# Optimization experiments

Hardware: AMD Instinct MI355X
Metric: run time of the kernel (lower is better)

Reference implementation:

```python
import jax, jax.numpy as jnp
import numpy as np

NUM_EXPERTS = 8
TOP_K = 2


def setup_inputs() -> dict:
    key = jax.random.key(0)
    ks = jax.random.split(key, 5)
    B, S, D, F, E = 4, 2048, 1024, 3584, NUM_EXPERTS
    scale = 0.02
    return {
        "hidden_states": jax.random.normal(ks[0], (B, S, D), dtype=jnp.float32),
        "gate_w": jax.random.normal(ks[1], (E, D), dtype=jnp.float32) * scale,
        "w1": jax.random.normal(ks[2], (E, D, F), dtype=jnp.float32) * scale,
        "w3": jax.random.normal(ks[3], (E, D, F), dtype=jnp.float32) * scale,
        "w2": jax.random.normal(ks[4], (E, F, D), dtype=jnp.float32) * scale,
    }


def reference(hidden_states, gate_w, w1, w3, w2):
    B, S, D = hidden_states.shape
    E = gate_w.shape[0]
    x = hidden_states.reshape(-1, D)  # [T, D]

    # Router: logits -> softmax -> top-k -> renormalize
    router_logits = x @ gate_w.T  # [T, E]
    routing_probs = jax.nn.softmax(router_logits, axis=-1)
    top_w, top_idx = jax.lax.top_k(routing_probs, TOP_K)  # [T, K]
    top_w = top_w / jnp.sum(top_w, axis=-1, keepdims=True)

    # Per-token weight for each expert (0 if not selected): [T, E]
    expert_weight = jnp.sum(
        jax.nn.one_hot(top_idx, E, dtype=x.dtype) * top_w[..., None], axis=1
    )

    # Dense masked dispatch: small fixed loop over experts (E=8), SwiGLU MLP.
    out = jnp.zeros_like(x)
    for e in range(E):
        h = jax.nn.silu(x @ w1[e]) * (x @ w3[e])  # [T, F]
        out = out + expert_weight[:, e:e + 1] * (h @ w2[e])  # [T, D]

    return out.reshape(B, S, D), router_logits
```

## Files before the change

kernel.cpp:

```cpp
#include <hip/hip_runtime.h>
#include <stdint.h>

#define T_TOKENS 8192
#define DDIM 1024
#define FDIM 3584
#define NEXP 8

#define BM 128
#define BK 64
#define MAXRT (T_TOKENS / BM)
#define H_ROWS (2 * T_TOKENS + BM)

typedef _Float16 f16x8 __attribute__((ext_vector_type(8)));
typedef _Float16 f16x4 __attribute__((ext_vector_type(4)));
typedef float f32x4 __attribute__((ext_vector_type(4)));

__device__ __forceinline__ void gload16(const void* g, void* l) {
  __builtin_amdgcn_global_load_lds(
      (const __attribute__((address_space(1))) void*)g,
      (__attribute__((address_space(3))) void*)l, 16, 0, 0);
}

__global__ __launch_bounds__(256) void router_kernel(
    const float* __restrict__ x, const float* __restrict__ gw,
    float* __restrict__ logits_out, int* __restrict__ counts,
    int* __restrict__ tok_idx, float* __restrict__ tok_w) {
  int t = blockIdx.x * 4 + (threadIdx.x >> 6);
  int lane = threadIdx.x & 63;
  const float* xr = x + (size_t)t * DDIM;
  float acc[NEXP];
#pragma unroll
  for (int e = 0; e < NEXP; e++) acc[e] = 0.f;
  for (int c = 0; c < DDIM / 64; c++) {
    float xv = xr[c * 64 + lane];
#pragma unroll
    for (int e = 0; e < NEXP; e++) acc[e] += xv * gw[e * DDIM + c * 64 + lane];
  }
#pragma unroll
  for (int e = 0; e < NEXP; e++) {
    for (int off = 32; off > 0; off >>= 1) acc[e] += __shfl_xor(acc[e], off, 64);
  }
  if (lane == 0) {
    float m = acc[0];
    for (int e = 1; e < NEXP; e++) m = fmaxf(m, acc[e]);
    float p[NEXP];
    for (int e = 0; e < NEXP; e++) p[e] = expf(acc[e] - m);
    int e1 = 0;
    for (int e = 1; e < NEXP; e++) if (p[e] > p[e1]) e1 = e;
    int e2 = (e1 == 0) ? 1 : 0;
    for (int e = 0; e < NEXP; e++) { if (e == e1) continue; if (p[e] > p[e2]) e2 = e; }
    float wsum = p[e1] + p[e2];
    float w1v = p[e1] / wsum, w2v = p[e2] / wsum;
    for (int e = 0; e < NEXP; e++) logits_out[(size_t)t * NEXP + e] = acc[e];
    int pos1 = atomicAdd(&counts[e1], 1);
    tok_idx[e1 * T_TOKENS + pos1] = t; tok_w[e1 * T_TOKENS + pos1] = w1v;
    int pos2 = atomicAdd(&counts[e2], 1);
    tok_idx[e2 * T_TOKENS + pos2] = t; tok_w[e2 * T_TOKENS + pos2] = w2v;
  }
}

__global__ void prefix_kernel(const int* __restrict__ counts, int* __restrict__ offsets) {
  if (threadIdx.x == 0) {
    int s = 0;
    for (int e = 0; e < NEXP; e++) { offsets[e] = s; s += counts[e]; }
    offsets[NEXP] = s;
  }
}

__global__ __launch_bounds__(256) void convert_x_kernel(const float* __restrict__ x,
                                                        _Float16* __restrict__ xh) {
  int i = blockIdx.x * 256 + threadIdx.x;
  const float4* s = (const float4*)x + (size_t)i * 2;
  float4 a = s[0], b = s[1];
  f16x8 o = {(_Float16)a.x, (_Float16)a.y, (_Float16)a.z, (_Float16)a.w,
             (_Float16)b.x, (_Float16)b.y, (_Float16)b.z, (_Float16)b.w};
  *((f16x8*)xh + i) = o;
}

__global__ __launch_bounds__(256) void transpose_f16_kernel(
    const float* __restrict__ in, _Float16* __restrict__ out, int R, int C) {
  __shared__ _Float16 lt[64][72];
  size_t esz = (size_t)R * C;
  in += blockIdx.z * esz;
  out += blockIdx.z * esz;
  int r0 = blockIdx.y * 64, c0 = blockIdx.x * 64;
  int t = threadIdx.x;
  int r = t >> 2, cs = (t & 3) * 16;
  const float* src = in + (size_t)(r0 + r) * C + c0 + cs;
#pragma unroll
  for (int q = 0; q < 4; q++) {
    float4 v = ((const float4*)src)[q];
    lt[cs + q * 4 + 0][r] = (_Float16)v.x;
    lt[cs + q * 4 + 1][r] = (_Float16)v.y;
    lt[cs + q * 4 + 2][r] = (_Float16)v.z;
    lt[cs + q * 4 + 3][r] = (_Float16)v.w;
  }
  __syncthreads();
  int cl = t >> 2, rs = (t & 3) * 16;
  _Float16* dst = out + (size_t)(c0 + cl) * R + r0 + rs;
#pragma unroll
  for (int q = 0; q < 2; q++)
    *(f16x8*)(dst + q * 8) = *(const f16x8*)&lt[cl][rs + q * 8];
}

__global__ __launch_bounds__(256) void gemm1_kernel(
    const _Float16* __restrict__ xh, const _Float16* __restrict__ w1t,
    const _Float16* __restrict__ w3t, const int* __restrict__ counts,
    const int* __restrict__ offsets, const int* __restrict__ tok_idx,
    _Float16* __restrict__ h) {
  int e = blockIdx.z;
  int cnt = counts[e];
  int rt = blockIdx.y;
  if (rt * BM >= cnt) return;
  int ct = blockIdx.x;
  int off = offsets[e];

  __shared__ _Float16 lA[BM * 64];
  __shared__ _Float16 lB1[64 * 64];
  __shared__ _Float16 lB3[64 * 64];

  int tid = threadIdx.x, lane = tid & 63, w = tid >> 6;
  int p = lane & 7;
  int rsub = lane >> 3;
  int c = p ^ rsub;

  const _Float16* aG[4];
  _Float16* aL[4];
#pragma unroll
  for (int g = 0; g < 4; g++) {
    int r = w * 32 + g * 8 + rsub;
    int ir = rt * BM + r;
    if (ir >= cnt) ir = cnt - 1;
    int tok = tok_idx[e * T_TOKENS + ir];
    aG[g] = xh + (size_t)tok * DDIM + c * 8;
    aL[g] = lA + (w * 32 + g * 8) * 64;
  }
  const _Float16 *b1G[2], *b3G[2];
  _Float16 *b1L[2], *b3L[2];
#pragma unroll
  for (int g = 0; g < 2; g++) {
    int n = w * 16 + g * 8 + rsub;
    size_t row = (size_t)e * FDIM + (size_t)ct * 64 + n;
    b1G[g] = w1t + row * DDIM + c * 8;
    b3G[g] = w3t + row * DDIM + c * 8;
    b1L[g] = lB1 + (w * 16 + g * 8) * 64;
    b3L[g] = lB3 + (w * 16 + g * 8) * 64;
  }

  f32x4 acc1[2][4], acc3[2][4];
  f32x4 zero = {0.f, 0.f, 0.f, 0.f};
#pragma unroll
  for (int i = 0; i < 2; i++)
#pragma unroll
    for (int j = 0; j < 4; j++) { acc1[i][j] = zero; acc3[i][j] = zero; }

  int wm = w * 32;
  int l15 = lane & 15;
  int qv = lane >> 4;
  int x7 = l15 & 7;

  for (int kt = 0; kt < DDIM / BK; kt++) {
#pragma unroll
    for (int g = 0; g < 4; g++) { gload16(aG[g], aL[g]); aG[g] += 64; }
#pragma unroll
    for (int g = 0; g < 2; g++) {
      gload16(b1G[g], b1L[g]); b1G[g] += 64;
      gload16(b3G[g], b3L[g]); b3G[g] += 64;
    }
    __syncthreads();
#pragma unroll
    for (int kk = 0; kk < 2; kk++) {
      int pc = (kk * 4 + qv) ^ x7;
      f16x8 af[2], b1f[4], b3f[4];
#pragma unroll
      for (int i = 0; i < 2; i++)
        af[i] = *(const f16x8*)&lA[(wm + i * 16 + l15) * 64 + pc * 8];
#pragma unroll
      for (int j = 0; j < 4; j++) {
        b1f[j] = *(const f16x8*)&lB1[(j * 16 + l15) * 64 + pc * 8];
        b3f[j] = *(const f16x8*)&lB3[(j * 16 + l15) * 64 + pc * 8];
      }
#pragma unroll
      for (int i = 0; i < 2; i++)
#pragma unroll
        for (int j = 0; j < 4; j++) {
          acc1[i][j] = __builtin_amdgcn_mfma_f32_16x16x32_f16(af[i], b1f[j], acc1[i][j], 0, 0, 0);
          acc3[i][j] = __builtin_amdgcn_mfma_f32_16x16x32_f16(af[i], b3f[j], acc3[i][j], 0, 0, 0);
        }
    }
    __syncthreads();
  }
  int q4 = qv * 4;
#pragma unroll
  for (int i = 0; i < 2; i++) {
#pragma unroll
    for (int r = 0; r < 4; r++) {
      int row = rt * BM + wm + i * 16 + q4 + r;
      if (row >= cnt) continue;
      _Float16* hrow = h + (size_t)(off + row) * FDIM + (size_t)ct * 64;
#pragma unroll
      for (int j = 0; j < 4; j++) {
        float a = acc1[i][j][r];
        float b = acc3[i][j][r];
        float hv = (a / (1.f + __expf(-a))) * b;
        hrow[j * 16 + l15] = (_Float16)hv;
      }
    }
  }
}

__global__ __launch_bounds__(256) void gemm2_kernel(
    const _Float16* __restrict__ h, const _Float16* __restrict__ w2t,
    const int* __restrict__ counts, const int* __restrict__ offsets,
    const int* __restrict__ tok_idx, const float* __restrict__ tok_w,
    float* __restrict__ out) {
  int e = blockIdx.z;
  int cnt = counts[e];
  int rt = blockIdx.y;
  if (rt * BM >= cnt) return;
  int ct = blockIdx.x;
  int off = offsets[e];

  __shared__ _Float16 lA[BM * 64];
  __shared__ _Float16 lB[128 * 64];

  int tid = threadIdx.x, lane = tid & 63, w = tid >> 6;
  int p = lane & 7;
  int rsub = lane >> 3;
  int c = p ^ rsub;

  const _Float16 *aG[4], *bG[4];
  _Float16 *aL[4], *bL[4];
#pragma unroll
  for (int g = 0; g < 4; g++) {
    int r = w * 32 + g * 8 + rsub;
    aG[g] = h + (size_t)(off + rt * BM + r) * FDIM + c * 8;
    aL[g] = lA + (w * 32 + g * 8) * 64;
    size_t row = (size_t)e * DDIM + (size_t)ct * 128 + r;
    bG[g] = w2t + row * FDIM + c * 8;
    bL[g] = lB + (w * 32 + g * 8) * 64;
  }

  f32x4 acc[2][8];
  f32x4 zero = {0.f, 0.f, 0.f, 0.f};
#pragma unroll
  for (int i = 0; i < 2; i++)
#pragma unroll
    for (int j = 0; j < 8; j++) acc[i][j] = zero;

  int wm = w * 32;
  int l15 = lane & 15;
  int qv = lane >> 4;
  int x7 = l15 & 7;

  for (int kt = 0; kt < FDIM / BK; kt++) {
#pragma unroll
    for (int g = 0; g < 4; g++) {
      gload16(aG[g], aL[g]); aG[g] += 64;
      gload16(bG[g], bL[g]); bG[g] += 64;
    }
    __syncthreads();
#pragma unroll
    for (int kk = 0; kk < 2; kk++) {
      int pc = (kk * 4 + qv) ^ x7;
      f16x8 af[2], bf[8];
#pragma unroll
      for (int i = 0; i < 2; i++)
        af[i] = *(const f16x8*)&lA[(wm + i * 16 + l15) * 64 + pc * 8];
#pragma unroll
      for (int j = 0; j < 8; j++)
        bf[j] = *(const f16x8*)&lB[(j * 16 + l15) * 64 + pc * 8];
#pragma unroll
      for (int i = 0; i < 2; i++)
#pragma unroll
        for (int j = 0; j < 8; j++)
          acc[i][j] = __builtin_amdgcn_mfma_f32_16x16x32_f16(af[i], bf[j], acc[i][j], 0, 0, 0);
    }
    __syncthreads();
  }
  int q4 = qv * 4;
#pragma unroll
  for (int i = 0; i < 2; i++) {
#pragma unroll
    for (int r = 0; r < 4; r++) {
      int row = rt * BM + wm + i * 16 + q4 + r;
      if (row >= cnt) continue;
      int t = tok_idx[e * T_TOKENS + row];
      float wgt = tok_w[e * T_TOKENS + row];
      float* orow = out + (size_t)t * DDIM + (size_t)ct * 128;
#pragma unroll
      for (int j = 0; j < 8; j++)
        atomicAdd(&orow[j * 16 + l15], acc[i][j][r] * wgt);
    }
  }
}

extern "C" void kernel_launch(void* const* d_in, const int* in_sizes, int n_in,
                              void* d_out, int out_size, void* d_ws, size_t ws_size,
                              hipStream_t stream) {
  const float* x  = (const float*)d_in[0];
  const float* gw = (const float*)d_in[1];
  const float* w1 = (const float*)d_in[2];
  const float* w3 = (const float*)d_in[3];
  const float* w2 = (const float*)d_in[4];
  float* out = (float*)d_out;
  float* logits = out + (size_t)T_TOKENS * DDIM;

  char* ws = (char*)d_ws;
  const size_t MB = 1024 * 1024;
  int* counts  = (int*)ws;
  int* offsets = (int*)(ws + 64);
  int* tok_idx = (int*)(ws + 256);
  float* tok_w = (float*)(ws + 256 + (size_t)NEXP * T_TOKENS * 4);
  _Float16* xh  = (_Float16*)(ws + 1 * MB);
  _Float16* w1t = (_Float16*)(ws + 17 * MB);
  _Float16* w3t = (_Float16*)(ws + 73 * MB);
  _Float16* w2t = (_Float16*)(ws + 129 * MB);
  _Float16* h   = (_Float16*)(ws + 185 * MB);

  hipMemsetAsync(counts, 0, 256, stream);
  hipMemsetAsync(out, 0, (size_t)T_TOKENS * DDIM * 4, stream);

  convert_x_kernel<<<T_TOKENS * DDIM / 8 / 256, 256, 0, stream>>>(x, xh);
  transpose_f16_kernel<<<dim3(FDIM / 64, DDIM / 64, NEXP), 256, 0, stream>>>(w1, w1t, DDIM, FDIM);
  transpose_f16_kernel<<<dim3(FDIM / 64, DDIM / 64, NEXP), 256, 0, stream>>>(w3, w3t, DDIM, FDIM);
  transpose_f16_kernel<<<dim3(DDIM / 64, FDIM / 64, NEXP), 256, 0, stream>>>(w2, w2t, FDIM, DDIM);

  router_kernel<<<T_TOKENS / 4, 256, 0, stream>>>(x, gw, logits, counts, tok_idx, tok_w);
  prefix_kernel<<<1, 64, 0, stream>>>(counts, offsets);

  gemm1_kernel<<<dim3(FDIM / 64, MAXRT, NEXP), 256, 0, stream>>>(xh, w1t, w3t, counts, offsets, tok_idx, h);
  gemm2_kernel<<<dim3(DDIM / 128, MAXRT, NEXP), 256, 0, stream>>>(h, w2t, counts, offsets, tok_idx, tok_w, out);
}
```

Before: 1.149 ms.

## Compact MoE tile schedule, replace atomic scatter with fp16 partials plus gather

Builds a compact list of (expert, row-tile) pairs in the prefix kernel, so the GEMM grids launch only up to 136 tiles instead of 8x64 mostly-empty blocks. Replaces per-element float atomicAdd scatter in gemm2 with fp16 partial rows written per assignment, then a gather kernel sums each token's two contributions. This also removes the output memset. Fuses the x-to-fp16 conversion into the router and reworks the transpose thread mapping. The partial sums are rounded to fp16 before the final add, which adds precision loss, plus an extra pass over the partial buffer.

New measurement: 1.140 ms. No clear change (-0.8%).

```diff
diff --git a/kernel.cpp b/kernel.cpp
--- a/kernel.cpp
+++ b/kernel.cpp
@@ -8,11 +8,9 @@
 
 #define BM 128
 #define BK 64
-#define MAXRT (T_TOKENS / BM)
-#define H_ROWS (2 * T_TOKENS + BM)
+#define MAXTT 136
 
 typedef _Float16 f16x8 __attribute__((ext_vector_type(8)));
-typedef _Float16 f16x4 __attribute__((ext_vector_type(4)));
 typedef float f32x4 __attribute__((ext_vector_type(4)));
 
 __device__ __forceinline__ void gload16(const void* g, void* l) {
@@ -24,7 +22,8 @@
 __global__ __launch_bounds__(256) void router_kernel(
     const float* __restrict__ x, const float* __restrict__ gw,
     float* __restrict__ logits_out, int* __restrict__ counts,
-    int* __restrict__ tok_idx, float* __restrict__ tok_w) {
+    int* __restrict__ tok_idx, float* __restrict__ tok_w,
+    int2* __restrict__ tok_ref, _Float16* __restrict__ xh) {
   int t = blockIdx.x * 4 + (threadIdx.x >> 6);
   int lane = threadIdx.x & 63;
   const float* xr = x + (size_t)t * DDIM;
@@ -33,6 +32,7 @@
   for (int e = 0; e < NEXP; e++) acc[e] = 0.f;
   for (int c = 0; c < DDIM / 64; c++) {
     float xv = xr[c * 64 + lane];
+    xh[(size_t)t * DDIM + c * 64 + lane] = (_Float16)xv;
 #pragma unroll
     for (int e = 0; e < NEXP; e++) acc[e] += xv * gw[e * DDIM + c * 64 + lane];
   }
@@ -56,62 +56,62 @@
     tok_idx[e1 * T_TOKENS + pos1] = t; tok_w[e1 * T_TOKENS + pos1] = w1v;
     int pos2 = atomicAdd(&counts[e2], 1);
     tok_idx[e2 * T_TOKENS + pos2] = t; tok_w[e2 * T_TOKENS + pos2] = w2v;
-  }
-}
-
-__global__ void prefix_kernel(const int* __restrict__ counts, int* __restrict__ offsets) {
+    tok_ref[t] = make_int2((e1 << 13) | pos1, (e2 << 13) | pos2);
+  }
+}
+
+__global__ void prefix_kernel(const int* __restrict__ counts, int* __restrict__ offsets,
+                              int* __restrict__ sched) {
   if (threadIdx.x == 0) {
-    int s = 0;
-    for (int e = 0; e < NEXP; e++) { offsets[e] = s; s += counts[e]; }
+    int s = 0, nt = 0;
+    for (int e = 0; e < NEXP; e++) {
+      offsets[e] = s;
+      int c = counts[e];
+      int ntile = (c + BM - 1) / BM;
+      for (int i = 0; i < ntile; i++) sched[nt++] = (e << 16) | i;
+      s += c;
+    }
     offsets[NEXP] = s;
-  }
-}
-
-__global__ __launch_bounds__(256) void convert_x_kernel(const float* __restrict__ x,
-                                                        _Float16* __restrict__ xh) {
-  int i = blockIdx.x * 256 + threadIdx.x;
-  const float4* s = (const float4*)x + (size_t)i * 2;
-  float4 a = s[0], b = s[1];
-  f16x8 o = {(_Float16)a.x, (_Float16)a.y, (_Float16)a.z, (_Float16)a.w,
-             (_Float16)b.x, (_Float16)b.y, (_Float16)b.z, (_Float16)b.w};
-  *((f16x8*)xh + i) = o;
+    for (; nt < MAXTT; nt++) sched[nt] = -1;
+  }
 }
 
 __global__ __launch_bounds__(256) void transpose_f16_kernel(
     const float* __restrict__ in, _Float16* __restrict__ out, int R, int C) {
   __shared__ _Float16 lt[64][72];
   size_t esz = (size_t)R * C;
-  in += blockIdx.z * esz;
-  out += blockIdx.z * esz;
+  in += (size_t)blockIdx.z * esz;
+  out += (size_t)blockIdx.z * esz;
   int r0 = blockIdx.y * 64, c0 = blockIdx.x * 64;
   int t = threadIdx.x;
-  int r = t >> 2, cs = (t & 3) * 16;
-  const float* src = in + (size_t)(r0 + r) * C + c0 + cs;
-#pragma unroll
-  for (int q = 0; q < 4; q++) {
-    float4 v = ((const float4*)src)[q];
-    lt[cs + q * 4 + 0][r] = (_Float16)v.x;
-    lt[cs + q * 4 + 1][r] = (_Float16)v.y;
-    lt[cs + q * 4 + 2][r] = (_Float16)v.z;
-    lt[cs + q * 4 + 3][r] = (_Float16)v.w;
-  }
+  int r = t & 63, q = t >> 6;
+  const float* src = in + (size_t)(r0 + r) * C + c0 + q * 16;
+  float4 v0 = ((const float4*)src)[0];
+  float4 v1 = ((const float4*)src)[1];
+  float4 v2 = ((const float4*)src)[2];
+  float4 v3 = ((const float4*)src)[3];
+  _Float16 f[16] = {
+      (_Float16)v0.x, (_Float16)v0.y, (_Float16)v0.z, (_Float16)v0.w,
+      (_Float16)v1.x, (_Float16)v1.y, (_Float16)v1.z, (_Float16)v1.w,
+      (_Float16)v2.x, (_Float16)v2.y, (_Float16)v2.z, (_Float16)v2.w,
+      (_Float16)v3.x, (_Float16)v3.y, (_Float16)v3.z, (_Float16)v3.w};
+#pragma unroll
+  for (int j = 0; j < 16; j++) lt[q * 16 + j][r] = f[j];
   __syncthreads();
-  int cl = t >> 2, rs = (t & 3) * 16;
-  _Float16* dst = out + (size_t)(c0 + cl) * R + r0 + rs;
-#pragma unroll
-  for (int q = 0; q < 2; q++)
-    *(f16x8*)(dst + q * 8) = *(const f16x8*)&lt[cl][rs + q * 8];
+  _Float16* dst = out + (size_t)(c0 + r) * R + r0 + q * 16;
+  *(f16x8*)dst       = *(const f16x8*)&lt[r][q * 16];
+  *(f16x8*)(dst + 8) = *(const f16x8*)&lt[r][q * 16 + 8];
 }
 
 __global__ __launch_bounds__(256) void gemm1_kernel(
     const _Float16* __restrict__ xh, const _Float16* __restrict__ w1t,
     const _Float16* __restrict__ w3t, const int* __restrict__ counts,
     const int* __restrict__ offsets, const int* __restrict__ tok_idx,
-    _Float16* __restrict__ h) {
-  int e = blockIdx.z;
+    const int* __restrict__ sched, _Float16* __restrict__ h) {
+  int sc = sched[blockIdx.y];
+  if (sc < 0) return;
+  int e = sc >> 16, rt = sc & 0xFFFF;
   int cnt = counts[e];
-  int rt = blockIdx.y;
-  if (rt * BM >= cnt) return;
   int ct = blockIdx.x;
   int off = offsets[e];
 
@@ -212,12 +212,12 @@
 __global__ __launch_bounds__(256) void gemm2_kernel(
     const _Float16* __restrict__ h, const _Float16* __restrict__ w2t,
     const int* __restrict__ counts, const int* __restrict__ offsets,
-    const int* __restrict__ tok_idx, const float* __restrict__ tok_w,
-    float* __restrict__ out) {
-  int e = blockIdx.z;
+    const float* __restrict__ tok_w, const int* __restrict__ sched,
+    _Float16* __restrict__ part) {
+  int sc = sched[blockIdx.y];
+  if (sc < 0) return;
+  int e = sc >> 16, rt = sc & 0xFFFF;
   int cnt = counts[e];
-  int rt = blockIdx.y;
-  if (rt * BM >= cnt) return;
   int ct = blockIdx.x;
   int off = offsets[e];
 
@@ -285,14 +285,29 @@
     for (int r = 0; r < 4; r++) {
       int row = rt * BM + wm + i * 16 + q4 + r;
       if (row >= cnt) continue;
-      int t = tok_idx[e * T_TOKENS + row];
       float wgt = tok_w[e * T_TOKENS + row];
-      float* orow = out + (size_t)t * DDIM + (size_t)ct * 128;
+      _Float16* prow = part + (size_t)(off + row) * DDIM + (size_t)ct * 128;
 #pragma unroll
       for (int j = 0; j < 8; j++)
-        atomicAdd(&orow[j * 16 + l15], acc[i][j][r] * wgt);
-    }
-  }
+        prow[j * 16 + l15] = (_Float16)(acc[i][j][r] * wgt);
+    }
+  }
+}
+
+__global__ __launch_bounds__(256) void gather_kernel(
+    const _Float16* __restrict__ part, const int2* __restrict__ tok_ref,
+    const int* __restrict__ offsets, float* __restrict__ out) {
+  int i = blockIdx.x * 256 + threadIdx.x;
+  int t = i >> 7;
+  int dc = (i & 127) * 8;
+  int2 ref = tok_ref[t];
+  int sa = offsets[ref.x >> 13] + (ref.x & 8191);
+  int sb = offsets[ref.y >> 13] + (ref.y & 8191);
+  f16x8 pa = *(const f16x8*)(part + (size_t)sa * DDIM + dc);
+  f16x8 pb = *(const f16x8*)(part + (size_t)sb * DDIM + dc);
+  float* dst = out + (size_t)t * DDIM + dc;
+#pragma unroll
+  for (int j = 0; j < 8; j++) dst[j] = (float)pa[j] + (float)pb[j];
 }
 
 extern "C" void kernel_launch(void* const* d_in, const int* in_sizes, int n_in,
@@ -310,25 +325,27 @@
   const size_t MB = 1024 * 1024;
   int* counts  = (int*)ws;
   int* offsets = (int*)(ws + 64);
-  int* tok_idx = (int*)(ws + 256);
-  float* tok_w = (float*)(ws + 256 + (size_t)NEXP * T_TOKENS * 4);
+  int* sched   = (int*)(ws + 128);
+  int* tok_idx = (int*)(ws + 1024);
+  float* tok_w = (float*)(ws + 1024 + 262144);
+  int2* tok_ref = (int2*)(ws + 1024 + 2 * 262144);
   _Float16* xh  = (_Float16*)(ws + 1 * MB);
   _Float16* w1t = (_Float16*)(ws + 17 * MB);
   _Float16* w3t = (_Float16*)(ws + 73 * MB);
   _Float16* w2t = (_Float16*)(ws + 129 * MB);
   _Float16* h   = (_Float16*)(ws + 185 * MB);
+  _Float16* part = (_Float16*)(ws + 304 * MB);
 
   hipMemsetAsync(counts, 0, 256, stream);
-  hipMemsetAsync(out, 0, (size_t)T_TOKENS * DDIM * 4, stream);
-
-  convert_x_kernel<<<T_TOKENS * DDIM / 8 / 256, 256, 0, stream>>>(x, xh);
+
+  router_kernel<<<T_TOKENS / 4, 256, 0, stream>>>(x, gw, logits, counts, tok_idx, tok_w, tok_ref, xh);
+  prefix_kernel<<<1, 64, 0, stream>>>(counts, offsets, sched);
+
   transpose_f16_kernel<<<dim3(FDIM / 64, DDIM / 64, NEXP), 256, 0, stream>>>(w1, w1t, DDIM, FDIM);
   transpose_f16_kernel<<<dim3(FDIM / 64, DDIM / 64, NEXP), 256, 0, stream>>>(w3, w3t, DDIM, FDIM);
   transpose_f16_kernel<<<dim3(DDIM / 64, FDIM / 64, NEXP), 256, 0, stream>>>(w2, w2t, FDIM, DDIM);
 
-  router_kernel<<<T_TOKENS / 4, 256, 0, stream>>>(x, gw, logits, counts, tok_idx, tok_w);
-  prefix_kernel<<<1, 64, 0, stream>>>(counts, offsets);
-
-  gemm1_kernel<<<dim3(FDIM / 64, MAXRT, NEXP), 256, 0, stream>>>(xh, w1t, w3t, counts, offsets, tok_idx, h);
-  gemm2_kernel<<<dim3(DDIM / 128, MAXRT, NEXP), 256, 0, stream>>>(h, w2t, counts, offsets, tok_idx, tok_w, out);
-}
+  gemm1_kernel<<<dim3(FDIM / 64, MAXTT), 256, 0, stream>>>(xh, w1t, w3t, counts, offsets, tok_idx, sched, h);
+  gemm2_kernel<<<dim3(DDIM / 128, MAXTT), 256, 0, stream>>>(h, w2t, counts, offsets, tok_w, sched, part);
+  gather_kernel<<<T_TOKENS * DDIM / 8 / 256, 256, 0, stream>>>(part, tok_ref, offsets, out);
+}
```
